# Optimization experiments

Measured on AMD Instinct MI355X. Metric: run time of the kernel, lower is better.

Reference implementation:

```python
import jax, jax.numpy as jnp
import numpy as np

HID = 128
NUM_HEADS = 8
NUM_LAYERS = 3
N_OP, N_MA, N_JOB = 50000, 1000, 5000
E_SIZES = [150000, 100000, 150000, 100000, 100000]
# (src_type, dst_type) for the 5 edge relations, in module order:
# precedence, assigned_to, can_process, contains, belongs_to
EDGE_SD = [("operation", "operation"), ("operation", "machine"), ("machine", "operation"), ("job", "operation"), ("operation", "job")]
NT_IDX = {"operation": 0, "machine": 1, "job": 2}


def setup_inputs() -> dict:
    key = jax.random.key(0)
    ks = list(jax.random.split(key, 80))
    it = iter(ks)

    def nrm(shape, scale=1.0):
        return jax.random.normal(next(it), shape, dtype=jnp.float32) * scale

    n_nodes = {"operation": N_OP, "machine": N_MA, "job": N_JOB}
    inp = {}
    inp["x_operation"] = nrm((N_OP, 64))
    inp["x_machine"] = nrm((N_MA, 32))
    inp["x_job"] = nrm((N_JOB, 16))
    ei_names = ["ei_prec", "ei_assign", "ei_canproc", "ei_contains", "ei_belongs"]
    ea_names = ["ea_prec", "ea_assign", "ea_canproc", "ea_contains", "ea_belongs"]
    for ne, na, E, (st, dt) in zip(ei_names, ea_names, E_SIZES, EDGE_SD):
        src = jax.random.randint(next(it), (E,), 0, n_nodes[st], dtype=jnp.int32)
        dst = jax.random.randint(next(it), (E,), 0, n_nodes[dt], dtype=jnp.int32)
        inp[ne] = jnp.stack([src, dst])
        inp[na] = nrm((E, 32))
    # node input projections (per-type dims)
    inp["Wn_op"] = nrm((64, HID), 64 ** -0.5)
    inp["bn_op"] = jnp.zeros((HID,), jnp.float32)
    inp["Wn_ma"] = nrm((32, HID), 32 ** -0.5)
    inp["bn_ma"] = jnp.zeros((HID,), jnp.float32)
    inp["Wn_job"] = nrm((16, HID), 16 ** -0.5)
    inp["bn_job"] = jnp.zeros((HID,), jnp.float32)
    # edge attr projections: 5 relations, 32 -> HID, applied once before the layers
    inp["We_proj"] = nrm((5, 32, HID), 32 ** -0.5)
    inp["be_proj"] = jnp.zeros((5, HID), jnp.float32)
    # GATConv params stacked as [layer, edge_type, ...]; heads*out == HID at every layer
    inp["Wg"] = nrm((NUM_LAYERS, 5, HID, HID), HID ** -0.5)      # shared lin for src/dst
    inp["att_s"] = nrm((NUM_LAYERS, 5, HID), HID ** -0.5)
    inp["att_d"] = nrm((NUM_LAYERS, 5, HID), HID ** -0.5)
    inp["Wge"] = nrm((NUM_LAYERS, 5, HID, HID), HID ** -0.5)     # lin_edge
    inp["att_e"] = nrm((NUM_LAYERS, 5, HID), HID ** -0.5)
    inp["bg"] = jnp.zeros((NUM_LAYERS, 5, HID), jnp.float32)      # GATConv output bias
    # BatchNorm affine: [layer, node_type, HID]
    inp["gamma"] = jnp.ones((NUM_LAYERS, 3, HID), jnp.float32)
    inp["beta"] = jnp.zeros((NUM_LAYERS, 3, HID), jnp.float32)
    # output projection for 'operation'
    inp["Wo"] = nrm((HID, HID), HID ** -0.5)
    inp["bo"] = jnp.zeros((HID,), jnp.float32)
    return inp


def _segment_softmax(logits, seg, num):
    # PyG softmax: exp(x - segment_max) / (segment_sum + 1e-16)
    m = jax.ops.segment_max(logits, seg, num_segments=num)
    m = jnp.where(jnp.isfinite(m), m, 0.0)  # empty segments -> 0
    ex = jnp.exp(logits - m[seg])
    den = jax.ops.segment_sum(ex, seg, num_segments=num)
    return ex / (den[seg] + 1e-16)


def _gat_forward(x_operation, x_machine, x_job, eis, eas_raw,
                 Wn_op, bn_op, Wn_ma, bn_ma, Wn_job, bn_job,
                 We_proj, be_proj, Wg, att_s, att_d, Wge, att_e, bg,
                 gamma, beta, Wo, bo):
    x = {
        "operation": x_operation @ Wn_op + bn_op,
        "machine": x_machine @ Wn_ma + bn_ma,
        "job": x_job @ Wn_job + bn_job,
    }
    # edge attrs projected once to HID
    eas = [eas_raw[t] @ We_proj[t] + be_proj[t] for t in range(5)]

    for i in range(NUM_LAYERS):
        H = NUM_HEADS if i < NUM_LAYERS - 1 else 1
        C = HID // H
        resid = x
        agg = {nt: jnp.zeros((x[nt].shape[0], HID), x[nt].dtype) for nt in x}
        for t, (st, dt) in enumerate(EDGE_SD):
            src, dst = eis[t][0], eis[t][1]
            n_dst = x[dt].shape[0]
            xs = (x[st] @ Wg[i, t]).reshape(-1, H, C)            # [Ns,H,C]
            xd = (x[dt] @ Wg[i, t]).reshape(-1, H, C)            # [Nd,H,C]
            a_s = (xs * att_s[i, t].reshape(H, C)).sum(-1)       # [Ns,H]
            a_d = (xd * att_d[i, t].reshape(H, C)).sum(-1)       # [Nd,H]
            e = (eas[t] @ Wge[i, t]).reshape(-1, H, C)           # [E,H,C]
            a_e = (e * att_e[i, t].reshape(H, C)).sum(-1)        # [E,H]
            logits = jax.nn.leaky_relu(a_s[src] + a_d[dst] + a_e, 0.2)
            alpha = _segment_softmax(logits, dst, n_dst)         # [E,H]
            msg = xs[src] * alpha[:, :, None]                    # [E,H,C]
            out = jax.ops.segment_sum(msg, dst, num_segments=n_dst)
            agg[dt] = agg[dt] + out.reshape(n_dst, HID) + bg[i, t]
        new_x = {}
        for nt in x:
            h = agg[nt]
            mu = h.mean(0)
            var = ((h - mu) ** 2).mean(0)  # biased, as BatchNorm1d training
            h = (h - mu) * jax.lax.rsqrt(var + 1e-5) * gamma[i, NT_IDX[nt]] + beta[i, NT_IDX[nt]]
            if i < NUM_LAYERS - 1:
                h = jax.nn.relu(h)  # dropout is identity in eval
            new_x[nt] = h + resid[nt]  # residual (dims always match: HID)
        x = new_x
    return x["operation"] @ Wo + bo


def reference(x_operation, x_machine, x_job,
              ei_prec, ei_assign, ei_canproc, ei_contains, ei_belongs,
              ea_prec, ea_assign, ea_canproc, ea_contains, ea_belongs,
              Wn_op, bn_op, Wn_ma, bn_ma, Wn_job, bn_job,
              We_proj, be_proj, Wg, att_s, att_d, Wge, att_e, bg,
              gamma, beta, Wo, bo):
    eis = [ei_prec, ei_assign, ei_canproc, ei_contains, ei_belongs]
    eas = [ea_prec, ea_assign, ea_canproc, ea_contains, ea_belongs]
    return _gat_forward(x_operation, x_machine, x_job, eis, eas,
                        Wn_op, bn_op, Wn_ma, bn_ma, Wn_job, bn_job,
                        We_proj, be_proj, Wg, att_s, att_d, Wge, att_e, bg,
                        gamma, beta, Wo, bo)
```

## Files before the change

### kernel.cpp

```cpp
#include <hip/hip_runtime.h>
#include <cstdint>

#define HID 128

static constexpr int kNOp = 50000, kNMa = 1000, kNJob = 5000;
static constexpr int kNTot = 56000;
static constexpr int kETot = 600000;
static constexpr int kSeg = 156000;
static constexpr int kEsz[5]   = {150000, 100000, 150000, 100000, 100000};
static constexpr int kSrcT[5]  = {0, 0, 1, 2, 0};
static constexpr int kDstT[5]  = {0, 1, 0, 0, 2};
static constexpr int kNodeOff[3] = {0, 50000, 51000};
static constexpr int kEoff[6]  = {0, 150000, 250000, 400000, 500000, 600000};
static constexpr int kRoff[5]  = {0, 50000, 100000, 101000, 106000};
static constexpr int kRTot = 156000;

typedef __attribute__((ext_vector_type(8))) __bf16 bf16x8;
typedef __attribute__((ext_vector_type(4))) float f32x4;

__device__ inline unsigned short f2b(float f) {
  unsigned u = __float_as_uint(f);
  unsigned r = (u + 0x7FFFu + ((u >> 16) & 1u)) >> 16;
  return (unsigned short)r;
}
__device__ inline float b2f(unsigned short u) {
  return __uint_as_float(((unsigned)u) << 16);
}

__device__ inline int seg_of(int t, int d) {
  if (t == 0) return 3 * d;
  if (t == 2) return 3 * d + 1;
  if (t == 3) return 3 * d + 2;
  if (t == 1) return 150000 + d;
  return 151000 + d;
}

__global__ void conv_pad(const float* __restrict__ in, unsigned short* __restrict__ out,
                         int M, int K, int Kp) {
  int i = blockIdx.x * blockDim.x + threadIdx.x;
  if (i >= M * Kp) return;
  int r = i / Kp, c = i - r * Kp;
  out[i] = (c < K) ? f2b(in[(size_t)r * K + c]) : (unsigned short)0;
}

__global__ void transpose_w(const float* __restrict__ W, unsigned short* __restrict__ Wt,
                            int K, int N, int Kp, int nmat) {
  int i = blockIdx.x * blockDim.x + threadIdx.x;
  int per = N * Kp;
  if (i >= nmat * per) return;
  int b = i / per, rem = i - b * per;
  int n = rem / Kp, k = rem - n * Kp;
  Wt[i] = (k < K) ? f2b(W[(size_t)b * K * N + (size_t)k * N + n]) : (unsigned short)0;
}

template <int KC>
__global__ __launch_bounds__(256) void gemm_mfma(
    const unsigned short* __restrict__ A, const unsigned short* __restrict__ Bt,
    const float* __restrict__ bias, float* __restrict__ Cf,
    unsigned short* __restrict__ Cb, int M) {
  const int K = KC * 32;
  int w = blockIdx.x * 4 + (threadIdx.x >> 6);
  int m0 = w * 16;
  if (m0 >= M) return;
  int lane = threadIdx.x & 63;
  int l16 = lane & 15, quad = lane >> 4;
  int arow = m0 + l16; if (arow >= M) arow = M - 1;
  bf16x8 af[KC];
#pragma unroll
  for (int kc = 0; kc < KC; kc++) {
    int4 raw = *(const int4*)(A + (size_t)arow * K + kc * 32 + quad * 8);
    af[kc] = __builtin_bit_cast(bf16x8, raw);
  }
#pragma unroll
  for (int nt = 0; nt < 8; nt++) {
    int col = nt * 16 + l16;
    f32x4 acc = {0.f, 0.f, 0.f, 0.f};
#pragma unroll
    for (int kc = 0; kc < KC; kc++) {
      int4 braw = *(const int4*)(Bt + (size_t)col * K + kc * 32 + quad * 8);
      acc = __builtin_amdgcn_mfma_f32_16x16x32_bf16(
          af[kc], __builtin_bit_cast(bf16x8, braw), acc, 0, 0, 0);
    }
    float bv = bias ? bias[col] : 0.f;
#pragma unroll
    for (int r = 0; r < 4; r++) {
      int row = m0 + quad * 4 + r;
      if (row < M) {
        float v = acc[r] + bv;
        if (Cf) Cf[(size_t)row * HID + col] = v;
        if (Cb) Cb[(size_t)row * HID + col] = f2b(v);
      }
    }
  }
}

struct GemmJobs {
  const unsigned short* A[5];
  const unsigned short* Bt[5];
  unsigned short* Cb[5];
  int M[5];
  int bpref[6];
};

__global__ __launch_bounds__(256) void gemm_batched(GemmJobs J) {
  int b = blockIdx.x;
  int t = 0;
  while (t < 4 && b >= J.bpref[t + 1]) t++;
  const int M = J.M[t];
  int strip = (b - J.bpref[t]) * 4 + (threadIdx.x >> 6);
  int m0 = strip * 16;
  if (m0 >= M) return;
  int lane = threadIdx.x & 63;
  int l16 = lane & 15, quad = lane >> 4;
  const unsigned short* A = J.A[t];
  const unsigned short* Bt = J.Bt[t];
  unsigned short* Cb = J.Cb[t];
  int arow = m0 + l16; if (arow >= M) arow = M - 1;
  bf16x8 af[4];
#pragma unroll
  for (int kc = 0; kc < 4; kc++) {
    int4 raw = *(const int4*)(A + (size_t)arow * HID + kc * 32 + quad * 8);
    af[kc] = __builtin_bit_cast(bf16x8, raw);
  }
#pragma unroll
  for (int nt = 0; nt < 8; nt++) {
    int col = nt * 16 + l16;
    f32x4 acc = {0.f, 0.f, 0.f, 0.f};
#pragma unroll
    for (int kc = 0; kc < 4; kc++) {
      int4 braw = *(const int4*)(Bt + (size_t)col * HID + kc * 32 + quad * 8);
      acc = __builtin_amdgcn_mfma_f32_16x16x32_bf16(
          af[kc], __builtin_bit_cast(bf16x8, braw), acc, 0, 0, 0);
    }
#pragma unroll
    for (int r = 0; r < 4; r++) {
      int row = m0 + quad * 4 + r;
      if (row < M) Cb[(size_t)row * HID + col] = f2b(acc[r]);
    }
  }
}

template <int NCOL>
__global__ __launch_bounds__(256) void gemm_as(
    const unsigned short* __restrict__ A, const unsigned short* __restrict__ Bt,
    float* __restrict__ out, int M) {
  int w = blockIdx.x * 4 + (threadIdx.x >> 6);
  int m0 = w * 16;
  if (m0 >= M) return;
  int lane = threadIdx.x & 63;
  int l16 = lane & 15, quad = lane >> 4;
  int arow = m0 + l16; if (arow >= M) arow = M - 1;
  bf16x8 af[4];
#pragma unroll
  for (int kc = 0; kc < 4; kc++) {
    int4 raw = *(const int4*)(A + (size_t)arow * HID + kc * 32 + quad * 8);
    af[kc] = __builtin_bit_cast(bf16x8, raw);
  }
#pragma unroll
  for (int nt = 0; nt < NCOL / 16; nt++) {
    int col = nt * 16 + l16;
    f32x4 acc = {0.f, 0.f, 0.f, 0.f};
#pragma unroll
    for (int kc = 0; kc < 4; kc++) {
      int4 braw = *(const int4*)(Bt + (size_t)col * HID + kc * 32 + quad * 8);
      acc = __builtin_amdgcn_mfma_f32_16x16x32_bf16(
          af[kc], __builtin_bit_cast(bf16x8, braw), acc, 0, 0, 0);
    }
#pragma unroll
    for (int r = 0; r < 4; r++) {
      int row = m0 + quad * 4 + r;
      if (row < M) out[(size_t)row * NCOL + col] = acc[r];
    }
  }
}

__global__ void fold_kernel(const float* __restrict__ Wg, const float* __restrict__ att_s,
                            const float* __restrict__ att_d, const float* __restrict__ Wge,
                            const float* __restrict__ att_e, const float* __restrict__ Wep,
                            const float* __restrict__ bep,
                            float* __restrict__ S, float* __restrict__ D,
                            float* __restrict__ w32, float* __restrict__ cvec) {
  int idx = blockIdx.x;
  int h = idx & 7, lt = idx >> 3;
  int l = lt / 5;
  int H = (l < 2) ? 8 : 1, C = HID / H;
  if (h >= H) return;
  int k = threadIdx.x;
  int t = lt % 5;
  const float* wg  = Wg  + (size_t)lt * HID * HID;
  const float* wge = Wge + (size_t)lt * HID * HID;
  const float* as_ = att_s + (size_t)lt * HID + h * C;
  const float* ad_ = att_d + (size_t)lt * HID + h * C;
  const float* ae_ = att_e + (size_t)lt * HID + h * C;
  float s = 0.f, d = 0.f, v = 0.f;
  for (int c = 0; c < C; c++) {
    float wr = wg[(size_t)k * HID + h * C + c];
    s += wr * as_[c];
    d += wr * ad_[c];
    v += wge[(size_t)k * HID + h * C + c] * ae_[c];
  }
  S[(size_t)idx * HID + k] = s;
  D[(size_t)idx * HID + k] = d;
  __shared__ float vs[HID];
  vs[k] = v;
  __syncthreads();
  if (k < 32) {
    const float* wp = Wep + (size_t)t * 32 * HID + (size_t)k * HID;
    float a = 0.f;
    for (int j = 0; j < HID; j++) a += wp[j] * vs[j];
    w32[(size_t)idx * 32 + k] = a;
  }
  if (k == 32) {
    const float* bp = bep + (size_t)t * HID;
    float a = 0.f;
    for (int j = 0; j < HID; j++) a += bp[j] * vs[j];
    cvec[idx] = a;
  }
}

__global__ void build_vb(const float* __restrict__ Sv, const float* __restrict__ Dv,
                         unsigned short* __restrict__ VbT) {
  int i = blockIdx.x * 256 + threadIdx.x;
  if (i >= 3 * 80 * HID) return;
  int l = i / (80 * HID), rem = i % (80 * HID);
  int col = rem / HID, k = rem % HID;
  int H = (l < 2) ? 8 : 1;
  float val = 0.f;
  if (col < 10 * H) {
    int v = col / H, h = col % H;
    const float* base = (v < 5) ? Sv : Dv;
    int t = (v < 5) ? v : v - 5;
    val = base[((size_t)(l * 5 + t) * 8 + h) * HID + k];
  }
  VbT[i] = f2b(val);
}

struct EdgeJobs {
  const int* src[5]; const int* dst[5];
};

__global__ void hist_b(EdgeJobs J, int* __restrict__ cnt) {
  int e = blockIdx.x * 256 + threadIdx.x;
  if (e >= kETot) return;
  int t = 0;
  while (t < 4 && e >= kEoff[t + 1]) t++;
  int d = J.dst[t][e - kEoff[t]];
  atomicAdd(&cnt[seg_of(t, d)], 1);
}

__global__ void scatter_b(EdgeJobs J, int* __restrict__ cursor,
                          int* __restrict__ perm, int* __restrict__ ssrc) {
  int e = blockIdx.x * 256 + threadIdx.x;
  if (e >= kETot) return;
  int t = 0;
  while (t < 4 && e >= kEoff[t + 1]) t++;
  int el = e - kEoff[t];
  int d = J.dst[t][el];
  int p = atomicAdd(&cursor[seg_of(t, d)], 1);
  perm[e] = p;
  ssrc[p] = J.src[t][el] + kRoff[t];
}

__global__ void scan_blocks(const int* __restrict__ in, int* __restrict__ out,
                            int* __restrict__ bsums, int n) {
  __shared__ int sh[256];
  int t = threadIdx.x;
  int base = blockIdx.x * 1024 + t * 4;
  int v[4]; int s = 0;
#pragma unroll
  for (int j = 0; j < 4; j++) { v[j] = (base + j < n) ? in[base + j] : 0; s += v[j]; }
  sh[t] = s;
  __syncthreads();
  for (int off = 1; off < 256; off <<= 1) {
    int x = (t >= off) ? sh[t - off] : 0;
    __syncthreads();
    sh[t] += x;
    __syncthreads();
  }
  int run = sh[t] - s;
#pragma unroll
  for (int j = 0; j < 4; j++) { if (base + j < n) out[base + j] = run; run += v[j]; }
  if (t == 255) bsums[blockIdx.x] = sh[255];
}

__global__ void scan_carry(int* bsums, int nb, int* sentinel) {
  if (threadIdx.x == 0 && blockIdx.x == 0) {
    int run = 0;
    for (int b = 0; b < nb; b++) { int x = bsums[b]; bsums[b] = run; run += x; }
    *sentinel = run;
  }
}

__global__ void scan_add(int* __restrict__ out, const int* __restrict__ bsums, int n) {
  int base = blockIdx.x * 1024 + threadIdx.x * 4;
  int c = bsums[blockIdx.x];
#pragma unroll
  for (int j = 0; j < 4; j++) if (base + j < n) out[base + j] += c;
}

__global__ void copy_k(const int* __restrict__ in, int* __restrict__ out, int n) {
  int i = blockIdx.x * blockDim.x + threadIdx.x;
  if (i < n) out[i] = in[i];
}

struct PassAJobs {
  const int* src[5]; const int* dst[5]; const int* perm[5];
  const float* ea[5];
  const float* w32[5]; const float* cv[5];
  int soff[5], doff[5];
  int E[5]; int bpref[6];
};

template <int H, int LD>
__global__ __launch_bounds__(256) void pass_a_b(PassAJobs J, const float* __restrict__ AS,
                                                float* __restrict__ logits) {
  int b = blockIdx.x;
  int t = 0;
  while (t < 4 && b >= J.bpref[t + 1]) t++;
  __shared__ float w[H][32];
  __shared__ float cc[H];
  for (int i = threadIdx.x; i < H * 32; i += 256) w[i >> 5][i & 31] = J.w32[t][i];
  if (threadIdx.x < H) cc[threadIdx.x] = J.cv[t][threadIdx.x];
  __syncthreads();
  int e = (b - J.bpref[t]) * 256 + threadIdx.x;
  if (e >= J.E[t]) return;
  int s = J.src[t][e], d = J.dst[t][e], pe = J.perm[t][e];
  const float* asp = AS + (size_t)(s + J.soff[t]) * LD + t * H;
  const float* adp = AS + (size_t)(d + J.doff[t]) * LD + (5 + t) * H;
  float x[32];
  const float4* p = (const float4*)(J.ea[t] + (size_t)e * 32);
#pragma unroll
  for (int i = 0; i < 8; i++) {
    float4 v = p[i];
    x[4 * i] = v.x; x[4 * i + 1] = v.y; x[4 * i + 2] = v.z; x[4 * i + 3] = v.w;
  }
#pragma unroll
  for (int h = 0; h < H; h++) {
    float a = cc[h];
#pragma unroll
    for (int k = 0; k < 32; k++) a += x[k] * w[h][k];
    float v = a + asp[h] + adp[h];
    v = v > 0.f ? v : 0.2f * v;
    logits[(size_t)pe * H + h] = v;
  }
}

template <int H>
__global__ void softmax_k(const int* __restrict__ rs, float* __restrict__ lg) {
  int g = (int)((blockIdx.x * (size_t)blockDim.x + threadIdx.x) >> 6);
  int lane = threadIdx.x & 63;
  if (g >= kSeg) return;
  int start = rs[g], end = rs[g + 1];
  int n = (end - start) * H;
  if (n == 0) return;
  float* L = lg + (size_t)start * H;
  float m = -3.0e38f;
  for (int idx = lane; idx < n; idx += 64) m = fmaxf(m, L[idx]);
  if (H == 8) {
    m = fmaxf(m, __shfl_xor(m, 8));
    m = fmaxf(m, __shfl_xor(m, 16));
    m = fmaxf(m, __shfl_xor(m, 32));
  } else {
#pragma unroll
    for (int off = 1; off < 64; off <<= 1) m = fmaxf(m, __shfl_xor(m, off));
  }
  float s = 0.f;
  for (int idx = lane; idx < n; idx += 64) {
    float ex = __expf(L[idx] - m);
    L[idx] = ex;
    s += ex;
  }
  if (H == 8) {
    s += __shfl_xor(s, 8);
    s += __shfl_xor(s, 16);
    s += __shfl_xor(s, 32);
  } else {
#pragma unroll
    for (int off = 1; off < 64; off <<= 1) s += __shfl_xor(s, off);
  }
  float inv = 1.f / (s + 1e-16f);
  for (int idx = lane; idx < n; idx += 64) L[idx] *= inv;
}

template <int H>
__global__ void gat_gather_u(const int* __restrict__ rs, const int* __restrict__ ssrc,
                             const float* __restrict__ alpha,
                             const unsigned short* __restrict__ xs,
                             float* __restrict__ agg) {
  int g = (int)((blockIdx.x * (size_t)blockDim.x + threadIdx.x) >> 6);
  int lane = threadIdx.x & 63;
  if (g >= kNTot) return;
  int start, end;
  if (g < 50000)      { start = rs[3 * g];              end = rs[3 * g + 3]; }
  else if (g < 51000) { int m = g - 50000; start = rs[150000 + m]; end = rs[150001 + m]; }
  else                { int j = g - 51000; start = rs[151000 + j]; end = rs[151001 + j]; }
  int deg = end - start;
  int l16 = lane & 15, quad = lane >> 4;
  int h = (H == 8) ? (l16 >> 1) : 0;
  float acc[8] = {0.f, 0.f, 0.f, 0.f, 0.f, 0.f, 0.f, 0.f};
  for (int base = 0; base < deg; base += 64) {
    int nchunk = deg - base; if (nchunk > 64) nchunk = 64;
    int sv = (lane < nchunk) ? ssrc[start + base + lane] : 0;
    for (int i = 0; i < nchunk; i += 4) {
      int e = i + quad;
      bool act = e < nchunk;
      int s = __shfl(sv, act ? e : 0);
      float w = act ? alpha[(size_t)(start + base + e) * H + h] : 0.f;
      int4 raw = *(const int4*)(xs + (size_t)s * HID + l16 * 8);
      unsigned ua[4] = {(unsigned)raw.x, (unsigned)raw.y, (unsigned)raw.z, (unsigned)raw.w};
#pragma unroll
      for (int j = 0; j < 4; j++) {
        acc[2 * j]     += w * __uint_as_float(ua[j] << 16);
        acc[2 * j + 1] += w * __uint_as_float(ua[j] & 0xFFFF0000u);
      }
    }
  }
#pragma unroll
  for (int j = 0; j < 8; j++) {
    acc[j] += __shfl_xor(acc[j], 16);
    acc[j] += __shfl_xor(acc[j], 32);
  }
  if (quad == 0) {
    float* p = agg + (size_t)g * HID + l16 * 8;
    *(float4*)p = make_float4(acc[0], acc[1], acc[2], acc[3]);
    *(float4*)(p + 4) = make_float4(acc[4], acc[5], acc[6], acc[7]);
  }
}

__global__ void colstats_b(const float* __restrict__ x, float* __restrict__ stats) {
  static constexpr int bpref[4] = {0, 384, 400, 448};
  static constexpr int rowoff[4] = {0, 50000, 51000, 56000};
  int b = blockIdx.x;
  int t = 0;
  while (t < 2 && b >= bpref[t + 1]) t++;
  int bl = b - bpref[t], nb = bpref[t + 1] - bpref[t];
  int tid = threadIdx.x;
  int col = tid & 127, half = tid >> 7;
  float s = 0.f, q = 0.f;
  for (int r = rowoff[t] + bl * 2 + half; r < rowoff[t + 1]; r += nb * 2) {
    float v = x[(size_t)r * HID + col];
    s += v; q += v * v;
  }
  __shared__ float ls[256], lq[256];
  ls[tid] = s; lq[tid] = q;
  __syncthreads();
  if (tid < 128) {
    s = ls[tid] + ls[tid + 128];
    q = lq[tid] + lq[tid + 128];
    unsafeAtomicAdd(&stats[t * 256 + col], s);
    unsafeAtomicAdd(&stats[t * 256 + 128 + col], q);
  }
}

__global__ void bn_apply_b(float* __restrict__ agg, const float* __restrict__ xold,
                           unsigned short* __restrict__ xnb, const float* __restrict__ stats,
                           const float* __restrict__ gammaL, const float* __restrict__ betaL,
                           int relu) {
  size_t i = blockIdx.x * (size_t)blockDim.x + threadIdx.x;
  if (i >= (size_t)kNTot * 32) return;
  int row = (int)(i >> 5);
  int t = (row < 50000) ? 0 : (row < 51000 ? 1 : 2);
  float invN = (t == 0) ? (1.f / 50000.f) : (t == 1 ? (1.f / 1000.f) : (1.f / 5000.f));
  const float* st = stats + t * 256;
  const float* gm = gammaL + t * HID;
  const float* bt = betaL + t * HID;
  int c4 = ((int)(i & 31)) * 4;
  float4 av = ((const float4*)agg)[i];
  float4 xv = ((const float4*)xold)[i];
  float a[4] = {av.x, av.y, av.z, av.w};
  float xo[4] = {xv.x, xv.y, xv.z, xv.w};
  float o[4];
#pragma unroll
  for (int j = 0; j < 4; j++) {
    int c = c4 + j;
    float mu = st[c] * invN;
    float var = st[128 + c] * invN - mu * mu;
    float g = gm[c] * rsqrtf(var + 1e-5f);
    float v = (a[j] - mu) * g + bt[c];
    if (relu) v = fmaxf(v, 0.f);
    o[j] = v + xo[j];
  }
  ((float4*)agg)[i] = make_float4(o[0], o[1], o[2], o[3]);
  ((ushort4*)xnb)[i] = make_ushort4(f2b(o[0]), f2b(o[1]), f2b(o[2]), f2b(o[3]));
}

extern "C" void kernel_launch(void* const* d_in, const int* in_sizes, int n_in,
                              void* d_out, int out_size, void* d_ws, size_t ws_size,
                              hipStream_t stream) {
  const float* x_in[3] = {(const float*)d_in[0], (const float*)d_in[1], (const float*)d_in[2]};
  const int* ei[5];
  const float* ea[5];
  for (int t = 0; t < 5; t++) {
    ei[t] = (const int*)d_in[3 + 2 * t];
    ea[t] = (const float*)d_in[4 + 2 * t];
  }
  const float* Wn[3]  = {(const float*)d_in[13], (const float*)d_in[15], (const float*)d_in[17]};
  const float* bnb[3] = {(const float*)d_in[14], (const float*)d_in[16], (const float*)d_in[18]};
  const float* Wep   = (const float*)d_in[19];
  const float* bep   = (const float*)d_in[20];
  const float* Wg    = (const float*)d_in[21];
  const float* att_s = (const float*)d_in[22];
  const float* att_d = (const float*)d_in[23];
  const float* Wge   = (const float*)d_in[24];
  const float* att_e = (const float*)d_in[25];
  const float* gamma = (const float*)d_in[27];
  const float* beta  = (const float*)d_in[28];
  const float* Wo    = (const float*)d_in[29];
  const float* bo    = (const float*)d_in[30];

  float* ws = (float*)d_ws;
  size_t off = 0;
  auto alloc = [&](size_t n) { size_t o = off; off += (n + 255) & ~(size_t)255; return o; };
  auto allocb = [&](size_t n) { return alloc((n + 1) / 2); };

  float* bufA = ws + alloc((size_t)kNTot * HID);
  float* bufB = ws + alloc((size_t)kNTot * HID);
  unsigned short* xcurb = (unsigned short*)(ws + allocb((size_t)kNTot * HID));
  unsigned short* xs_all = (unsigned short*)(ws + allocb((size_t)kRTot * HID));
  unsigned short* WgT  = (unsigned short*)(ws + allocb((size_t)15 * HID * HID));
  unsigned short* WoT  = (unsigned short*)(ws + allocb((size_t)HID * HID));
  unsigned short* WnT_op  = (unsigned short*)(ws + allocb((size_t)HID * 64));
  unsigned short* WnT_ma  = (unsigned short*)(ws + allocb((size_t)HID * 32));
  unsigned short* WnT_job = (unsigned short*)(ws + allocb((size_t)HID * 32));
  unsigned short* VbT  = (unsigned short*)(ws + allocb((size_t)3 * 80 * HID));
  float* Sv     = ws + alloc((size_t)15 * 8 * HID);
  float* Dv     = ws + alloc((size_t)15 * 8 * HID);
  float* w32    = ws + alloc((size_t)15 * 8 * 32);
  float* cv     = ws + alloc((size_t)15 * 8);
  float* stats  = ws + alloc((size_t)3 * 256);
  float* ASbuf  = ws + alloc((size_t)kNTot * 80);
  float* logits = ws + alloc((size_t)kETot * 8 + 64);
  int* rs_all   = (int*)(ws + alloc((size_t)kSeg + 8));
  int* perm_all = (int*)(ws + alloc((size_t)kETot));
  int* ssrc_all = (int*)(ws + alloc((size_t)kETot));
  unsigned short* xinb_op  = xs_all;
  unsigned short* xinb_ma  = xs_all + 3200000;
  unsigned short* xinb_job = xs_all + 3232000;
  int* cnt    = (int*)logits;
  int* cursor = (int*)(logits + 156032);
  int* bsums  = (int*)(logits + 312064);
  (void)ws_size; (void)in_sizes; (void)n_in; (void)out_size;

  float* xcur = bufA;
  float* agg  = bufB;

  EdgeJobs EJ;
  for (int t = 0; t < 5; t++) { EJ.src[t] = ei[t]; EJ.dst[t] = ei[t] + kEsz[t]; }
  hipMemsetAsync(cnt, 0, (size_t)kSeg * 4, stream);
  hist_b<<<(kETot + 255) / 256, 256, 0, stream>>>(EJ, cnt);
  int nb = (kSeg + 1023) / 1024;
  scan_blocks<<<nb, 256, 0, stream>>>(cnt, rs_all, bsums, kSeg);
  scan_carry<<<1, 64, 0, stream>>>(bsums, nb, rs_all + kSeg);
  scan_add<<<nb, 256, 0, stream>>>(rs_all, bsums, kSeg);
  copy_k<<<(kSeg + 255) / 256, 256, 0, stream>>>(rs_all, cursor, kSeg);
  scatter_b<<<(kETot + 255) / 256, 256, 0, stream>>>(EJ, cursor, perm_all, ssrc_all);

  conv_pad<<<(kNOp * 64 + 255) / 256, 256, 0, stream>>>(x_in[0], xinb_op, kNOp, 64, 64);
  conv_pad<<<(kNMa * 32 + 255) / 256, 256, 0, stream>>>(x_in[1], xinb_ma, kNMa, 32, 32);
  conv_pad<<<(kNJob * 32 + 255) / 256, 256, 0, stream>>>(x_in[2], xinb_job, kNJob, 16, 32);
  transpose_w<<<(HID * 64 + 255) / 256, 256, 0, stream>>>(Wn[0], WnT_op, 64, HID, 64, 1);
  transpose_w<<<(HID * 32 + 255) / 256, 256, 0, stream>>>(Wn[1], WnT_ma, 32, HID, 32, 1);
  transpose_w<<<(HID * 32 + 255) / 256, 256, 0, stream>>>(Wn[2], WnT_job, 16, HID, 32, 1);
  transpose_w<<<(15 * HID * HID + 255) / 256, 256, 0, stream>>>(Wg, WgT, HID, HID, HID, 15);
  transpose_w<<<(HID * HID + 255) / 256, 256, 0, stream>>>(Wo, WoT, HID, HID, HID, 1);
  fold_kernel<<<120, 128, 0, stream>>>(Wg, att_s, att_d, Wge, att_e, Wep, bep,
                                       Sv, Dv, w32, cv);
  build_vb<<<(3 * 80 * HID + 255) / 256, 256, 0, stream>>>(Sv, Dv, VbT);

  gemm_mfma<2><<<((kNOp + 15) / 16 + 3) / 4, 256, 0, stream>>>(
      xinb_op, WnT_op, bnb[0], xcur, xcurb, kNOp);
  gemm_mfma<1><<<((kNMa + 15) / 16 + 3) / 4, 256, 0, stream>>>(
      xinb_ma, WnT_ma, bnb[1], xcur + (size_t)50000 * HID, xcurb + (size_t)50000 * HID, kNMa);
  gemm_mfma<1><<<((kNJob + 15) / 16 + 3) / 4, 256, 0, stream>>>(
      xinb_job, WnT_job, bnb[2], xcur + (size_t)51000 * HID, xcurb + (size_t)51000 * HID, kNJob);

  static constexpr int gemmBpref[6]  = {0, 782, 1564, 1580, 1659, 2441};
  static constexpr int passABpref[6] = {0, 587, 978, 1565, 1956, 2347};
  static constexpr int nsRel[5] = {50000, 50000, 1000, 5000, 50000};

  for (int l = 0; l < 3; l++) {
    int H = (l < 2) ? 8 : 1;

    GemmJobs GJ;
    for (int t = 0; t < 5; t++) {
      int lt = l * 5 + t;
      GJ.A[t]  = xcurb + (size_t)kNodeOff[kSrcT[t]] * HID;
      GJ.Bt[t] = WgT + (size_t)lt * HID * HID;
      GJ.Cb[t] = xs_all + (size_t)kRoff[t] * HID;
      GJ.M[t] = nsRel[t];
      GJ.bpref[t] = gemmBpref[t];
    }
    GJ.bpref[5] = gemmBpref[5];
    gemm_batched<<<gemmBpref[5], 256, 0, stream>>>(GJ);

    int asBlocks = ((kNTot + 15) / 16 + 3) / 4;
    if (H == 8)
      gemm_as<80><<<asBlocks, 256, 0, stream>>>(xcurb, VbT + (size_t)l * 80 * HID, ASbuf, kNTot);
    else
      gemm_as<16><<<asBlocks, 256, 0, stream>>>(xcurb, VbT + (size_t)l * 80 * HID, ASbuf, kNTot);

    PassAJobs PJ;
    for (int t = 0; t < 5; t++) {
      int lt = l * 5 + t;
      PJ.src[t] = ei[t]; PJ.dst[t] = ei[t] + kEsz[t];
      PJ.perm[t] = perm_all + kEoff[t];
      PJ.ea[t] = ea[t];
      PJ.w32[t] = w32 + (size_t)lt * 8 * 32;
      PJ.cv[t]  = cv + (size_t)lt * 8;
      PJ.soff[t] = kNodeOff[kSrcT[t]];
      PJ.doff[t] = kNodeOff[kDstT[t]];
      PJ.E[t] = kEsz[t];
      PJ.bpref[t] = passABpref[t];
    }
    PJ.bpref[5] = passABpref[5];
    if (H == 8) pass_a_b<8, 80><<<passABpref[5], 256, 0, stream>>>(PJ, ASbuf, logits);
    else        pass_a_b<1, 16><<<passABpref[5], 256, 0, stream>>>(PJ, ASbuf, logits);

    if (H == 8) {
      softmax_k<8><<<((size_t)kSeg * 64 + 255) / 256, 256, 0, stream>>>(rs_all, logits);
      gat_gather_u<8><<<((size_t)kNTot * 64 + 255) / 256, 256, 0, stream>>>(
          rs_all, ssrc_all, logits, xs_all, agg);
    } else {
      softmax_k<1><<<((size_t)kSeg * 64 + 255) / 256, 256, 0, stream>>>(rs_all, logits);
      gat_gather_u<1><<<((size_t)kNTot * 64 + 255) / 256, 256, 0, stream>>>(
          rs_all, ssrc_all, logits, xs_all, agg);
    }

    hipMemsetAsync(stats, 0, 3 * 256 * 4, stream);
    colstats_b<<<448, 256, 0, stream>>>(agg, stats);
    bn_apply_b<<<(unsigned)(((size_t)kNTot * 32 + 255) / 256), 256, 0, stream>>>(
        agg, xcur, xcurb, stats, gamma + (size_t)l * 3 * HID, beta + (size_t)l * 3 * HID,
        (l < 2) ? 1 : 0);
    float* tmp = xcur; xcur = agg; agg = tmp;
  }

  gemm_mfma<4><<<((kNOp + 15) / 16 + 3) / 4, 256, 0, stream>>>(
      xcurb, WoT, bo, (float*)d_out, nullptr, kNOp);
}
```

Baseline: 1.038 ms.

## Precompute edge-attribute attention terms for all layers once, sorted by segment

The per-edge edge-attribute logit contribution (32-wide dot products with the folded weights) is computed for all three layers in a single pass before the layer loop and stored in destination-sorted order. Packed src/dst indices with the relation tag are also produced at scatter time. Per-layer pass A then becomes a pure sorted-order gather-add-LeakyReLU with coalesced logits writes instead of rereading edge attributes and scattering through perm. This costs extra workspace of about 17 floats per edge and one upfront kernel.

Result: faster. 1.003 ms (-3.4%).

```diff
diff --git a/kernel.cpp b/kernel.cpp
--- a/kernel.cpp
+++ b/kernel.cpp
@@ -11,6 +11,8 @@
 static constexpr int kSrcT[5]  = {0, 0, 1, 2, 0};
 static constexpr int kDstT[5]  = {0, 1, 0, 0, 2};
 static constexpr int kNodeOff[3] = {0, 50000, 51000};
+static constexpr int kSoff[5]  = {0, 0, 50000, 51000, 0};
+static constexpr int kDoff[5]  = {0, 50000, 0, 0, 51000};
 static constexpr int kEoff[6]  = {0, 150000, 250000, 400000, 500000, 600000};
 static constexpr int kRoff[5]  = {0, 50000, 100000, 101000, 106000};
 static constexpr int kRTot = 156000;
@@ -249,16 +251,20 @@
 }
 
 __global__ void scatter_b(EdgeJobs J, int* __restrict__ cursor,
-                          int* __restrict__ perm, int* __restrict__ ssrc) {
+                          int* __restrict__ perm, int* __restrict__ ssrc,
+                          int* __restrict__ spack, int* __restrict__ dpack) {
   int e = blockIdx.x * 256 + threadIdx.x;
   if (e >= kETot) return;
   int t = 0;
   while (t < 4 && e >= kEoff[t + 1]) t++;
   int el = e - kEoff[t];
+  int s = J.src[t][el];
   int d = J.dst[t][el];
   int p = atomicAdd(&cursor[seg_of(t, d)], 1);
   perm[e] = p;
-  ssrc[p] = J.src[t][el] + kRoff[t];
+  ssrc[p] = s + kRoff[t];
+  spack[p] = ((s + kSoff[t]) << 3) | t;
+  dpack[p] = ((d + kDoff[t]) << 3) | t;
 }
 
 __global__ void scan_blocks(const int* __restrict__ in, int* __restrict__ out,
@@ -303,46 +309,103 @@
   if (i < n) out[i] = in[i];
 }
 
-struct PassAJobs {
-  const int* src[5]; const int* dst[5]; const int* perm[5];
+struct FoldAeJobs {
   const float* ea[5];
-  const float* w32[5]; const float* cv[5];
-  int soff[5], doff[5];
+  const int* perm[5];
   int E[5]; int bpref[6];
 };
 
-template <int H, int LD>
-__global__ __launch_bounds__(256) void pass_a_b(PassAJobs J, const float* __restrict__ AS,
-                                                float* __restrict__ logits) {
+__global__ __launch_bounds__(256) void fold_ae(FoldAeJobs J, const float* __restrict__ w32,
+                                               const float* __restrict__ cv,
+                                               float* __restrict__ ae0, float* __restrict__ ae1,
+                                               float* __restrict__ ae2) {
   int b = blockIdx.x;
   int t = 0;
   while (t < 4 && b >= J.bpref[t + 1]) t++;
-  __shared__ float w[H][32];
-  __shared__ float cc[H];
-  for (int i = threadIdx.x; i < H * 32; i += 256) w[i >> 5][i & 31] = J.w32[t][i];
-  if (threadIdx.x < H) cc[threadIdx.x] = J.cv[t][threadIdx.x];
+  __shared__ float w[3][8][32];
+  __shared__ float cc[3][8];
+  for (int i = threadIdx.x; i < 3 * 8 * 32; i += 256) {
+    int l = i >> 8, rem = i & 255;
+    w[l][rem >> 5][rem & 31] = w32[(size_t)((l * 5 + t) * 8) * 32 + rem];
+  }
+  if (threadIdx.x < 24) {
+    int l = threadIdx.x >> 3, h = threadIdx.x & 7;
+    cc[l][h] = cv[(size_t)(l * 5 + t) * 8 + h];
+  }
   __syncthreads();
   int e = (b - J.bpref[t]) * 256 + threadIdx.x;
   if (e >= J.E[t]) return;
-  int s = J.src[t][e], d = J.dst[t][e], pe = J.perm[t][e];
-  const float* asp = AS + (size_t)(s + J.soff[t]) * LD + t * H;
-  const float* adp = AS + (size_t)(d + J.doff[t]) * LD + (5 + t) * H;
   float x[32];
-  const float4* p = (const float4*)(J.ea[t] + (size_t)e * 32);
+  const float4* p4 = (const float4*)(J.ea[t] + (size_t)e * 32);
 #pragma unroll
   for (int i = 0; i < 8; i++) {
-    float4 v = p[i];
+    float4 v = p4[i];
     x[4 * i] = v.x; x[4 * i + 1] = v.y; x[4 * i + 2] = v.z; x[4 * i + 3] = v.w;
   }
-#pragma unroll
-  for (int h = 0; h < H; h++) {
-    float a = cc[h];
-#pragma unroll
-    for (int k = 0; k < 32; k++) a += x[k] * w[h][k];
-    float v = a + asp[h] + adp[h];
-    v = v > 0.f ? v : 0.2f * v;
-    logits[(size_t)pe * H + h] = v;
-  }
+  int p = J.perm[t][e];
+  float o[8];
+#pragma unroll
+  for (int h = 0; h < 8; h++) {
+    float a = cc[0][h];
+#pragma unroll
+    for (int k = 0; k < 32; k++) a += x[k] * w[0][h][k];
+    o[h] = a;
+  }
+  float4* d0 = (float4*)(ae0 + (size_t)p * 8);
+  d0[0] = make_float4(o[0], o[1], o[2], o[3]);
+  d0[1] = make_float4(o[4], o[5], o[6], o[7]);
+#pragma unroll
+  for (int h = 0; h < 8; h++) {
+    float a = cc[1][h];
+#pragma unroll
+    for (int k = 0; k < 32; k++) a += x[k] * w[1][h][k];
+    o[h] = a;
+  }
+  float4* d1 = (float4*)(ae1 + (size_t)p * 8);
+  d1[0] = make_float4(o[0], o[1], o[2], o[3]);
+  d1[1] = make_float4(o[4], o[5], o[6], o[7]);
+  float a = cc[2][0];
+#pragma unroll
+  for (int k = 0; k < 32; k++) a += x[k] * w[2][0][k];
+  ae2[p] = a;
+}
+
+__global__ __launch_bounds__(256) void pass_a8(const int* __restrict__ spack,
+                                               const int* __restrict__ dpack,
+                                               const float* __restrict__ ae,
+                                               const float* __restrict__ AS,
+                                               float* __restrict__ logits) {
+  int p = blockIdx.x * 256 + threadIdx.x;
+  if (p >= kETot) return;
+  int sv = spack[p], dv = dpack[p];
+  int t = sv & 7;
+  const float4* asp = (const float4*)(AS + (size_t)(sv >> 3) * 80 + t * 8);
+  const float4* adp = (const float4*)(AS + (size_t)(dv >> 3) * 80 + (5 + t) * 8);
+  const float4* aep = (const float4*)(ae + (size_t)p * 8);
+  float4 s0 = asp[0], s1 = asp[1];
+  float4 d0 = adp[0], d1 = adp[1];
+  float4 e0 = aep[0], e1 = aep[1];
+  float v[8] = {s0.x + d0.x + e0.x, s0.y + d0.y + e0.y, s0.z + d0.z + e0.z, s0.w + d0.w + e0.w,
+                s1.x + d1.x + e1.x, s1.y + d1.y + e1.y, s1.z + d1.z + e1.z, s1.w + d1.w + e1.w};
+#pragma unroll
+  for (int j = 0; j < 8; j++) v[j] = v[j] > 0.f ? v[j] : 0.2f * v[j];
+  float4* L = (float4*)(logits + (size_t)p * 8);
+  L[0] = make_float4(v[0], v[1], v[2], v[3]);
+  L[1] = make_float4(v[4], v[5], v[6], v[7]);
+}
+
+__global__ __launch_bounds__(256) void pass_a1(const int* __restrict__ spack,
+                                               const int* __restrict__ dpack,
+                                               const float* __restrict__ ae2,
+                                               const float* __restrict__ AS,
+                                               float* __restrict__ logits) {
+  int p = blockIdx.x * 256 + threadIdx.x;
+  if (p >= kETot) return;
+  int sv = spack[p], dv = dpack[p];
+  int t = sv & 7;
+  float v = ae2[p] + AS[(size_t)(sv >> 3) * 16 + t] + AS[(size_t)(dv >> 3) * 16 + 5 + t];
+  v = v > 0.f ? v : 0.2f * v;
+  logits[p] = v;
 }
 
 template <int H>
@@ -533,6 +596,11 @@
   int* rs_all   = (int*)(ws + alloc((size_t)kSeg + 8));
   int* perm_all = (int*)(ws + alloc((size_t)kETot));
   int* ssrc_all = (int*)(ws + alloc((size_t)kETot));
+  int* spack    = (int*)(ws + alloc((size_t)kETot));
+  int* dpack    = (int*)(ws + alloc((size_t)kETot));
+  float* ae0    = ws + alloc((size_t)kETot * 8);
+  float* ae1    = ws + alloc((size_t)kETot * 8);
+  float* ae2    = ws + alloc((size_t)kETot);
   unsigned short* xinb_op  = xs_all;
   unsigned short* xinb_ma  = xs_all + 3200000;
   unsigned short* xinb_job = xs_all + 3232000;
@@ -553,7 +621,8 @@
   scan_carry<<<1, 64, 0, stream>>>(bsums, nb, rs_all + kSeg);
   scan_add<<<nb, 256, 0, stream>>>(rs_all, bsums, kSeg);
   copy_k<<<(kSeg + 255) / 256, 256, 0, stream>>>(rs_all, cursor, kSeg);
-  scatter_b<<<(kETot + 255) / 256, 256, 0, stream>>>(EJ, cursor, perm_all, ssrc_all);
+  scatter_b<<<(kETot + 255) / 256, 256, 0, stream>>>(EJ, cursor, perm_all, ssrc_all,
+                                                     spack, dpack);
 
   conv_pad<<<(kNOp * 64 + 255) / 256, 256, 0, stream>>>(x_in[0], xinb_op, kNOp, 64, 64);
   conv_pad<<<(kNMa * 32 + 255) / 256, 256, 0, stream>>>(x_in[1], xinb_ma, kNMa, 32, 32);
@@ -567,16 +636,26 @@
                                        Sv, Dv, w32, cv);
   build_vb<<<(3 * 80 * HID + 255) / 256, 256, 0, stream>>>(Sv, Dv, VbT);
 
+  static constexpr int gemmBpref[6]  = {0, 782, 1564, 1580, 1659, 2441};
+  static constexpr int foldBpref[6]  = {0, 587, 978, 1565, 1956, 2347};
+  static constexpr int nsRel[5] = {50000, 50000, 1000, 5000, 50000};
+
+  FoldAeJobs FJ;
+  for (int t = 0; t < 5; t++) {
+    FJ.ea[t] = ea[t];
+    FJ.perm[t] = perm_all + kEoff[t];
+    FJ.E[t] = kEsz[t];
+    FJ.bpref[t] = foldBpref[t];
+  }
+  FJ.bpref[5] = foldBpref[5];
+  fold_ae<<<foldBpref[5], 256, 0, stream>>>(FJ, w32, cv, ae0, ae1, ae2);
+
   gemm_mfma<2><<<((kNOp + 15) / 16 + 3) / 4, 256, 0, stream>>>(
       xinb_op, WnT_op, bnb[0], xcur, xcurb, kNOp);
   gemm_mfma<1><<<((kNMa + 15) / 16 + 3) / 4, 256, 0, stream>>>(
       xinb_ma, WnT_ma, bnb[1], xcur + (size_t)50000 * HID, xcurb + (size_t)50000 * HID, kNMa);
   gemm_mfma<1><<<((kNJob + 15) / 16 + 3) / 4, 256, 0, stream>>>(
       xinb_job, WnT_job, bnb[2], xcur + (size_t)51000 * HID, xcurb + (size_t)51000 * HID, kNJob);
-
-  static constexpr int gemmBpref[6]  = {0, 782, 1564, 1580, 1659, 2441};
-  static constexpr int passABpref[6] = {0, 587, 978, 1565, 1956, 2347};
-  static constexpr int nsRel[5] = {50000, 50000, 1000, 5000, 50000};
 
   for (int l = 0; l < 3; l++) {
     int H = (l < 2) ? 8 : 1;
@@ -599,22 +678,13 @@
     else
       gemm_as<16><<<asBlocks, 256, 0, stream>>>(xcurb, VbT + (size_t)l * 80 * HID, ASbuf, kNTot);
 
-    PassAJobs PJ;
-    for (int t = 0; t < 5; t++) {
-      int lt = l * 5 + t;
-      PJ.src[t] = ei[t]; PJ.dst[t] = ei[t] + kEsz[t];
-      PJ.perm[t] = perm_all + kEoff[t];
-      PJ.ea[t] = ea[t];
-      PJ.w32[t] = w32 + (size_t)lt * 8 * 32;
-      PJ.cv[t]  = cv + (size_t)lt * 8;
-      PJ.soff[t] = kNodeOff[kSrcT[t]];
-      PJ.doff[t] = kNodeOff[kDstT[t]];
-      PJ.E[t] = kEsz[t];
-      PJ.bpref[t] = passABpref[t];
-    }
-    PJ.bpref[5] = passABpref[5];
-    if (H == 8) pass_a_b<8, 80><<<passABpref[5], 256, 0, stream>>>(PJ, ASbuf, logits);
-    else        pass_a_b<1, 16><<<passABpref[5], 256, 0, stream>>>(PJ, ASbuf, logits);
+    int pblocks = (kETot + 255) / 256;
+    if (H == 8) {
+      const float* aeL = (l == 0) ? ae0 : ae1;
+      pass_a8<<<pblocks, 256, 0, stream>>>(spack, dpack, aeL, ASbuf, logits);
+    } else {
+      pass_a1<<<pblocks, 256, 0, stream>>>(spack, dpack, ae2, ASbuf, logits);
+    }
 
     if (H == 8) {
       softmax_k<8><<<((size_t)kSeg * 64 + 255) / 256, 256, 0, stream>>>(rs_all, logits);
```
